# Performance work log

Hardware: AMD Instinct MI355X
Metric: run time of the kernel (lower is better)

## Reference

```python
import jax, jax.numpy as jnp
import numpy as np

# ---- static configuration (mirrors init_kwargs) ----
B, V, C, NH, HD = 1, 6, 256, 8, 32     # batch, views, embed, heads, head_dim
Z, L, P = 4, 4, 2                       # z-ref points, fmap levels, ref points
BEV_H, BEV_W = 80, 80
Q = BEV_H * BEV_W
IMG_H, IMG_W = 480, 800
LEVEL_SHAPES = [(60, 100), (30, 50), (15, 25), (8, 13)]
S = sum(h * w for h, w in LEVEL_SHAPES)
RES = 0.512
OFFSET_SCALE = 1.0
FF = 512


def layer_norm(x, g, b):
    m = jnp.mean(x, -1, keepdims=True)
    v = jnp.var(x, -1, keepdims=True)
    return (x - m) / jnp.sqrt(v + 1e-5) * g + b


def _bev_grid():
    xs = (jnp.arange(BEV_W) + 0.5) / BEV_W
    ys = (jnp.arange(BEV_H) + 0.5) / BEV_H
    gy, gx = jnp.meshgrid(ys, xs, indexing='ij')
    ref = jnp.stack([gx.reshape(-1), gy.reshape(-1)], -1)        # (Q,2) normalized xy
    world = (ref - 0.5) * jnp.array([BEV_W * RES, BEV_H * RES])  # (Q,2) ego-frame meters
    return ref, world


def deform_sample(value, H, W, loc):
    """Bilinear sampling. value: (N, H*W, NH, HD); loc: (N, Qn, NH, PP, 2) in [0,1].
    Returns (N, Qn, NH, PP, HD); out-of-bounds samples contribute zero."""
    v = jnp.moveaxis(value, 2, 1)                                # (N, NH, HW, HD)
    x = loc[..., 0] * W - 0.5
    y = loc[..., 1] * H - 0.5
    x0 = jnp.floor(x); y0 = jnp.floor(y)
    lx, ly = x - x0, y - y0
    x0 = x0.astype(jnp.int32); y0 = y0.astype(jnp.int32)
    gather = jax.vmap(jax.vmap(lambda vt, it: vt[it]))           # over (N, NH)
    def corner(xi, yi, w):
        ok = ((xi >= 0) & (xi < W) & (yi >= 0) & (yi < H)).astype(value.dtype)
        idx = jnp.clip(yi, 0, H - 1) * W + jnp.clip(xi, 0, W - 1)
        g = gather(v, jnp.moveaxis(idx, 2, 1))                   # (N,NH,Qn,PP,HD)
        return jnp.moveaxis(g, 1, 2) * (w * ok)[..., None]
    return (corner(x0, y0, (1 - lx) * (1 - ly)) + corner(x0 + 1, y0, lx * (1 - ly))
            + corner(x0, y0 + 1, (1 - lx) * ly) + corner(x0 + 1, y0 + 1, lx * ly))


def _forward(bev_queries, bev_histories, multiscale_fmaps, transition_matrices, z_refs,
             cam_proj_matrices, Wv_t, Woff_t, boff_t, Ww_t, bw_t, Wo_t, bo_t, ln1_g, ln1_b,
             Wv_s, Woff_s, boff_s, Ww_s, bw_s, Wo_s, bo_s, ln2_g, ln2_b,
             W1, b1, W2, b2, ln3_g, ln3_b):
    ref, world = _bev_grid()
    q = bev_queries
    # ---------- temporal self-attention (deformable over current + warped history) ----------
    vcur = (q @ Wv_t).reshape(B, Q, NH, HD)
    vhist = (bev_histories @ Wv_t).reshape(B, Q, NH, HD)
    off_t = (q @ Woff_t + boff_t).reshape(B, Q, NH, 2, P, 2) * OFFSET_SCALE
    w_t = jax.nn.softmax((q @ Ww_t + bw_t).reshape(B, Q, NH, 2 * P), -1).reshape(B, Q, NH, 2, P)
    ext = jnp.array([BEV_W * RES, BEV_H * RES], jnp.float32)
    wh = jnp.concatenate([world, jnp.ones((Q, 1), jnp.float32)], -1)     # (Q,3)
    warped = jnp.einsum('bij,qj->bqi', transition_matrices, wh)          # (B,Q,3)
    ref_hist = warped[..., :2] / warped[..., 2:3] / ext + 0.5            # (B,Q,2)
    norm_bev = jnp.array([BEV_W, BEV_H], jnp.float32)
    loc_c = ref[None, :, None, None, :] + off_t[:, :, :, 0] / norm_bev
    loc_h = ref_hist[:, :, None, None, :] + off_t[:, :, :, 1] / norm_bev
    s_c = deform_sample(vcur, BEV_H, BEV_W, loc_c)                       # (B,Q,NH,P,HD)
    s_h = deform_sample(vhist, BEV_H, BEV_W, loc_h)
    out_t = (jnp.einsum('bqhp,bqhpd->bqhd', w_t[:, :, :, 0], s_c)
             + jnp.einsum('bqhp,bqhpd->bqhd', w_t[:, :, :, 1], s_h))
    out1 = out_t.reshape(B, Q, C) @ Wo_t + bo_t
    out2 = layer_norm(out1 + q, ln1_g, ln1_b)
    # ---------- spatial cross-attention (multi-view multi-scale deformable) ----------
    val = (multiscale_fmaps @ Wv_s).reshape(B * V, S, NH, HD)
    pts = jnp.concatenate([
        jnp.broadcast_to(world[:, None, :], (Q, Z, 2)),
        jnp.broadcast_to(z_refs[None, :, None], (Q, Z, 1)),
        jnp.ones((Q, Z, 1), jnp.float32)], -1)                           # (Q,Z,4) homogeneous
    uvd = jnp.einsum('vij,qzj->vqzi', cam_proj_matrices, pts)            # (V,Q,Z,3)
    d = uvd[..., 2]
    un = uvd[..., 0] / jnp.maximum(d, 1e-5) / IMG_W
    vn = uvd[..., 1] / jnp.maximum(d, 1e-5) / IMG_H
    valid = ((d > 1e-5) & (un >= 0) & (un <= 1) & (vn >= 0) & (vn <= 1)).astype(q.dtype)
    refuv = jnp.stack([un, vn], -1)                                      # (V,Q,Z,2)
    off_s = (out2 @ Woff_s + boff_s).reshape(B, Q, NH, Z, L, P, 2) * OFFSET_SCALE
    w_s = jax.nn.softmax((out2 @ Ww_s + bw_s).reshape(B, Q, NH, Z * L * P), -1)
    w_s = w_s.reshape(B, Q, NH, Z, L, P)
    acc = jnp.zeros((B, Q, NH, HD), q.dtype)
    start = 0
    for l, (Hl, Wl) in enumerate(LEVEL_SHAPES):
        vl = val[:, start:start + Hl * Wl]
        start += Hl * Wl
        loc = (refuv[None, :, :, None, :, None, :]
               + off_s[:, None, :, :, :, l] / jnp.array([Wl, Hl], jnp.float32))
        loc = jnp.broadcast_to(loc, (B, V, Q, NH, Z, P, 2)).reshape(B * V, Q, NH, Z * P, 2)
        samp = deform_sample(vl, Hl, Wl, loc).reshape(B, V, Q, NH, Z, P, HD)
        wl = w_s[:, None, :, :, :, l] * valid[None, :, :, None, :, None]
        acc = acc + jnp.einsum('bvqhzp,bvqhzpd->bqhd', wl, samp)
    count = jnp.maximum(valid.sum((0, 2)), 1.0)                          # (Q,) hit count
    out3 = (acc / count[None, :, None, None]).reshape(B, Q, C) @ Wo_s + bo_s
    out4 = layer_norm(out3 + out2, ln2_g, ln2_b)
    # ---------- feed-forward ----------
    out5 = jax.nn.relu(out4 @ W1 + b1) @ W2 + b2
    return layer_norm(out5 + out4, ln3_g, ln3_b)


def setup_inputs() -> dict:
    key = jax.random.key(0)
    ks = iter(jax.random.split(key, 40))
    def rn(shape, s=1.0):
        return jax.random.normal(next(ks), shape, jnp.float32) * s
    sc = 1.0 / float(np.sqrt(C))
    inp = {}
    inp['bev_queries'] = rn((B, Q, C), 0.1)
    inp['bev_histories'] = rn((B, Q, C), 0.1)
    inp['multiscale_fmaps'] = rn((B, V, S, C), 0.1)
    th = 0.02
    T = np.array([[np.cos(th), -np.sin(th), 0.5],
                  [np.sin(th), np.cos(th), 0.1],
                  [0.0, 0.0, 1.0]], np.float32)
    inp['transition_matrices'] = jnp.tile(jnp.asarray(T)[None], (B, 1, 1))
    inp['z_refs'] = jnp.linspace(-5.0, 3.0, Z).astype(jnp.float32)
    K = np.array([[400.0, 0.0, IMG_W / 2], [0.0, 400.0, IMG_H / 2], [0.0, 0.0, 1.0]], np.float32)
    Ps = []
    for vi in range(V):
        a = 2 * np.pi * vi / V
        Rt = np.zeros((3, 4), np.float32)
        Rt[0, :3] = [-np.sin(a), np.cos(a), 0.0]   # camera right
        Rt[1, :3] = [0.0, 0.0, -1.0]               # camera down
        Rt[2, :3] = [np.cos(a), np.sin(a), 0.0]    # camera forward
        Ps.append(K @ Rt)
    inp['cam_proj_matrices'] = jnp.asarray(np.stack(Ps))
    # temporal self-attention params
    inp['Wv_t'] = rn((C, C), sc)
    inp['Woff_t'] = rn((C, NH * 2 * P * 2), sc * 0.1)
    inp['boff_t'] = jnp.zeros((NH * 2 * P * 2,), jnp.float32)
    inp['Ww_t'] = rn((C, NH * 2 * P), sc)
    inp['bw_t'] = jnp.zeros((NH * 2 * P,), jnp.float32)
    inp['Wo_t'] = rn((C, C), sc)
    inp['bo_t'] = jnp.zeros((C,), jnp.float32)
    inp['ln1_g'] = jnp.ones((C,), jnp.float32)
    inp['ln1_b'] = jnp.zeros((C,), jnp.float32)
    # spatial cross-attention params
    inp['Wv_s'] = rn((C, C), sc)
    inp['Woff_s'] = rn((C, NH * Z * L * P * 2), sc * 0.1)
    inp['boff_s'] = jnp.zeros((NH * Z * L * P * 2,), jnp.float32)
    inp['Ww_s'] = rn((C, NH * Z * L * P), sc)
    inp['bw_s'] = jnp.zeros((NH * Z * L * P,), jnp.float32)
    inp['Wo_s'] = rn((C, C), sc)
    inp['bo_s'] = jnp.zeros((C,), jnp.float32)
    inp['ln2_g'] = jnp.ones((C,), jnp.float32)
    inp['ln2_b'] = jnp.zeros((C,), jnp.float32)
    # FFN params
    inp['W1'] = rn((C, FF), sc)
    inp['b1'] = jnp.zeros((FF,), jnp.float32)
    inp['W2'] = rn((FF, C), 1.0 / float(np.sqrt(FF)))
    inp['b2'] = jnp.zeros((C,), jnp.float32)
    inp['ln3_g'] = jnp.ones((C,), jnp.float32)
    inp['ln3_b'] = jnp.zeros((C,), jnp.float32)
    # static shape descriptors (treated as compile-time constants)
    inp['bev_spatial_shape'] = np.array([[BEV_H, BEV_W]], np.int64)
    inp['multiscale_fmap_shapes'] = np.array(LEVEL_SHAPES, np.int64)
    inp['img_spatial_shape'] = np.array([[IMG_H, IMG_W]], np.int64)
    return inp


def reference(bev_queries, bev_histories, multiscale_fmaps, transition_matrices, z_refs,
              cam_proj_matrices, Wv_t, Woff_t, boff_t, Ww_t, bw_t, Wo_t, bo_t, ln1_g, ln1_b,
              Wv_s, Woff_s, boff_s, Ww_s, bw_s, Wo_s, bo_s, ln2_g, ln2_b,
              W1, b1, W2, b2, ln3_g, ln3_b,
              bev_spatial_shape, multiscale_fmap_shapes, img_spatial_shape):
    return _forward(bev_queries, bev_histories, multiscale_fmaps, transition_matrices, z_refs,
                    cam_proj_matrices, Wv_t, Woff_t, boff_t, Ww_t, bw_t, Wo_t, bo_t, ln1_g, ln1_b,
                    Wv_s, Woff_s, boff_s, Ww_s, bw_s, Wo_s, bo_s, ln2_g, ln2_b,
                    W1, b1, W2, b2, ln3_g, ln3_b)
```

## Files before the change

### kernel.cpp

```cpp
#include <hip/hip_runtime.h>
#include <hip/hip_bf16.h>
#include <hip/hip_fp16.h>

typedef unsigned short u16;
typedef unsigned int u32;
typedef __attribute__((ext_vector_type(8))) _Float16 f16x8;
typedef __attribute__((ext_vector_type(4))) float f32x4;

#define Q_N  6400
#define S_N  7979
#define BEV  80

__device__ __forceinline__ float f16tof(u16 u) {
    __half h; *(u16*)&h = u; return __half2float(h);
}
__device__ __forceinline__ u16 ftof16(float f) {
    __half h = __float2half(f); return *(u16*)&h;
}

template <int AIN, int RELU, int OUTMODE, int SM4, int SM32>
__device__ __forceinline__ void gemm_body(
    const void* __restrict__ A, const u16* __restrict__ WT,
    const float* __restrict__ bias, const float* __restrict__ bias2,
    void* __restrict__ Cout, int M, int N, int K, int bx, int by,
// ... 60 lines not shown
        int col = n0 + wn + j * 16 + fr;
        if (bias2) bv[j] = (col < 512) ? bias[col] : bias2[col - 512];
        else       bv[j] = bias ? bias[col] : 0.f;
    }
    const bool do_sm4  = SM4 && (wn == 64);
    #pragma unroll
    for (int i = 0; i < 2; ++i) {
        #pragma unroll
        for (int r = 0; r < 4; ++r) {
            const int row = m0 + wm + i * 16 + g4r + r;
            float v0 = acc[i * 4 + 0][r] + bv[0];
            float v1 = acc[i * 4 + 1][r] + bv[1];
            float v2 = acc[i * 4 + 2][r] + bv[2];
            float v3 = acc[i * 4 + 3][r] + bv[3];
            if (RELU) {
                v0 = fmaxf(v0, 0.f); v1 = fmaxf(v1, 0.f);
                v2 = fmaxf(v2, 0.f); v3 = fmaxf(v3, 0.f);
            }
            if (SM4 && do_sm4) {
                float m0q = fmaxf(v0, __shfl_xor(v0, 1));
                m0q = fmaxf(m0q, __shfl_xor(m0q, 2));
                float e0 = __expf(v0 - m0q);
                float s0 = e0 + __shfl_xor(e0, 1);
                s0 += __shfl_xor(s0, 2);
                v0 = e0 / s0;
                float m1q = fmaxf(v1, __shfl_xor(v1, 1));
                m1q = fmaxf(m1q, __shfl_xor(m1q, 2));
                float e1 = __expf(v1 - m1q);
                float s1 = e1 + __shfl_xor(e1, 1);
                s1 += __shfl_xor(s1, 2);
                v1 = e1 / s1;
                v2 = 0.f; v3 = 0.f;
            }
            if (row < M) {
                const int colb = n0 + wn + fr;
                if (OUTMODE == 1) {
                    u16* cp = (u16*)Cout + (size_t)row * N;
                    cp[colb]      = ftof16(v0);
                    cp[colb + 16] = ftof16(v1);
                    cp[colb + 32] = ftof16(v2);
                    cp[colb + 48] = ftof16(v3);
                } else {
                    float* cp = (float*)Cout + (size_t)row * N;
                    cp[colb]      = v0;
                    cp[colb + 16] = v1;
                    cp[colb + 32] = v2;
                    cp[colb + 48] = v3;
                }
            }
        }
    }
}

__global__ __launch_bounds__(256) void fused3_k(
    const float* __restrict__ fmaps, const float* __restrict__ q, const float* __restrict__ hist,
    const u16* __restrict__ Wv_s_h, const u16* __restrict__ Wv_t_h,
    const u16* __restrict__ Wc_h, const float* __restrict__ bc,
    u16* __restrict__ val_f16, u16* __restrict__ vcur, u16* __restrict__ vhist,
    float* __restrict__ owt)
{
    __shared__ u16 Ah[64 * 40], Wh[128 * 40];
    const int b = blockIdx.x;
    if (b < 1498) {
        gemm_body<0, 0, 1, 0, 0>(fmaps, Wv_s_h, nullptr, nullptr, val_f16,
                                 47874, 256, 256, b & 1, b >> 1, Ah, Wh);
    } else if (b < 1698) {
        int l = b - 1498;
        gemm_body<0, 0, 1, 0, 0>(q, Wv_t_h, nullptr, nullptr, vcur,
                                 6400, 256, 256, l & 1, l >> 1, Ah, Wh);
    } else if (b < 1898) {
        int l = b - 1698;
        gemm_body<0, 0, 1, 0, 0>(hist, Wv_t_h, nullptr, nullptr, vhist,
                                 6400, 256, 256, l & 1, l >> 1, Ah, Wh);
    } else {
        int l = b - 1898;
        gemm_body<0, 0, 0, 1, 0>(q, Wc_h, bc, nullptr, owt,
                                 6400, 128, 256, 0, l, Ah, Wh);
    }
}

template <int AIN, int RELU, int OUTMODE, int SM32, int STATS, int LNA>
__global__ __launch_bounds__(256, 4) void cgemm_k(
    const void* __restrict__ A, const u16* __restrict__ WT,
    const float* __restrict__ bias, const float* __restrict__ bias2,
    const float* __restrict__ res, float* __restrict__ rstat,
    const float* __restrict__ lng, const float* __restrict__ lnb,
    float* __restrict__ aux,
    void* __restrict__ Cout, int M, int N, int K)
{
    __shared__ u16 As[2][32 * 40];
    __shared__ u16 Wsh[2][64 * 40];
    const int tid  = threadIdx.x;
    const int lane = tid & 63;
    const int wave = tid >> 6;
    const int wm = (wave >> 1) * 16, wn = (wave & 1) * 32;
    const int fr = lane & 15, g = lane >> 4;
    const int nx = gridDim.x;
    const int nwg = nx * gridDim.y;
    const int o = blockIdx.y * nx + blockIdx.x;
    const int flat = (o & 7) * (nwg >> 3) + (o >> 3);
    const int bx = flat % nx, by = flat / nx;
    const int m0 = by * 32, n0 = bx * 64;
    const int ar = tid >> 3, ak = (tid & 7) * 4;
    const int wr = tid >> 2, wk = (tid & 3) * 8;
    const int NS = K >> 5;

    f32x4 acc[2] = {(f32x4)(0.f), (f32x4)(0.f)};

    const float* apf = (const float*)A + (size_t)(m0 + ar) * K + ak;
    const u16*  aph  = (const u16*)A + (size_t)(m0 + ar) * K + ak;
    const u16*  wp   = WT + (size_t)(n0 + wr) * K + wk;

    const float* rp = nullptr;
    float* auxp = nullptr;
    float mean = 0.f, rstd = 0.f;
    if (LNA) {
        rp = res + (size_t)(m0 + ar) * 256 + ak;
        if (bx == 0) auxp = aux + (size_t)(m0 + ar) * 256 + ak;
        const float sm = rstat[m0 + ar];
        const float sq = rstat[Q_N + m0 + ar];
        mean = sm * (1.f / 256.f);
        rstd = rsqrtf(sq * (1.f / 256.f) - mean * mean + 1e-5f);
    }

    if (AIN == 0) {
        float4 v = *(const float4*)apf;
        if (LNA) {
            float4 rr = *(const float4*)rp;
            float4 gg = *(const float4*)(lng + ak);
            float4 bb = *(const float4*)(lnb + ak);
            v.x = (v.x + rr.x - mean) * rstd * gg.x + bb.x;
            v.y = (v.y + rr.y - mean) * rstd * gg.y + bb.y;
            v.z = (v.z + rr.z - mean) * rstd * gg.z + bb.z;
            v.w = (v.w + rr.w - mean) * rstd * gg.w + bb.w;
            if (auxp) *(float4*)auxp = v;
        }
        u16 hb[4];
        hb[0] = ftof16(v.x); hb[1] = ftof16(v.y); hb[2] = ftof16(v.z); hb[3] = ftof16(v.w);
        *(ushort4*)&As[0][ar * 40 + ak] = *(ushort4*)&hb[0];
    } else {
        *(uint2*)&As[0][ar * 40 + ak] = *(const uint2*)aph;
    }
    *(uint4*)&Wsh[0][wr * 40 + wk] = *(const uint4*)wp;
    __syncthreads();

    for (int s = 0; s < NS; ++s) {
        float4 av; float4 rv; uint2 au; uint4 wv;
        const bool pf = (s + 1) < NS;
        if (pf) {
            if (AIN == 0) {
                av = *(const float4*)(apf + (s + 1) * 32);
                if (LNA) rv = *(const float4*)(rp + (s + 1) * 32);
            } else {
                au = *(const uint2*)(aph + (s + 1) * 32);
            }
            wv = *(const uint4*)(wp + (s + 1) * 32);
        }
        const int b = s & 1;
        f16x8 fa  = *(const f16x8*)&As[b][(wm + fr) * 40 + g * 8];
        f16x8 fw0 = *(const f16x8*)&Wsh[b][(wn + fr) * 40 + g * 8];
        f16x8 fw1 = *(const f16x8*)&Wsh[b][(wn + 16 + fr) * 40 + g * 8];
        acc[0] = __builtin_amdgcn_mfma_f32_16x16x32_f16(fa, fw0, acc[0], 0, 0, 0);
        acc[1] = __builtin_amdgcn_mfma_f32_16x16x32_f16(fa, fw1, acc[1], 0, 0, 0);
        if (pf) {
            const int nb = b ^ 1;
            if (AIN == 0) {
                if (LNA) {
                    const int ko = ak + (s + 1) * 32;
                    float4 gg = *(const float4*)(lng + ko);
                    float4 bb = *(const float4*)(lnb + ko);
                    av.x = (av.x + rv.x - mean) * rstd * gg.x + bb.x;
                    av.y = (av.y + rv.y - mean) * rstd * gg.y + bb.y;
                    av.z = (av.z + rv.z - mean) * rstd * gg.z + bb.z;
                    av.w = (av.w + rv.w - mean) * rstd * gg.w + bb.w;
                    if (auxp) *(float4*)(auxp + (s + 1) * 32) = av;
                }
                u16 hb[4];
                hb[0] = ftof16(av.x); hb[1] = ftof16(av.y);
                hb[2] = ftof16(av.z); hb[3] = ftof16(av.w);
                *(ushort4*)&As[nb][ar * 40 + ak] = *(ushort4*)&hb[0];
            } else {
                *(uint2*)&As[nb][ar * 40 + ak] = au;
            }
            *(uint4*)&Wsh[nb][wr * 40 + wk] = wv;
        }
        __syncthreads();
    }

    const int c0g = n0 + wn + fr, c1g = c0g + 16;
    float bv0, bv1;
    if (bias2) {
        bv0 = (c0g < 512) ? bias[c0g] : bias2[c0g - 512];
        bv1 = (c1g < 512) ? bias[c1g] : bias2[c1g - 512];
    } else {
        bv0 = bias ? bias[c0g] : 0.f;
        bv1 = bias ? bias[c1g] : 0.f;
    }
    const bool do_sm32 = SM32 && ((n0 + wn) >= 512);
    #pragma unroll
    for (int r = 0; r < 4; ++r) {
        const int row = m0 + wm + g * 4 + r;
        float v0 = acc[0][r] + bv0;
        float v1 = acc[1][r] + bv1;
        if (RELU) { v0 = fmaxf(v0, 0.f); v1 = fmaxf(v1, 0.f); }
        if (SM32 && do_sm32) {
            float ma = fmaxf(v0, v1);
            ma = fmaxf(ma, __shfl_xor(ma, 1));
            ma = fmaxf(ma, __shfl_xor(ma, 2));
            ma = fmaxf(ma, __shfl_xor(ma, 4));
            ma = fmaxf(ma, __shfl_xor(ma, 8));
            float e0 = __expf(v0 - ma), e1 = __expf(v1 - ma);
            float sa = e0 + e1;
            sa += __shfl_xor(sa, 1);
            sa += __shfl_xor(sa, 2);
            sa += __shfl_xor(sa, 4);
            sa += __shfl_xor(sa, 8);
            float ia = 1.f / sa;
            v0 = e0 * ia; v1 = e1 * ia;
        }
        if (STATS) {
            float t0 = v0 + res[(size_t)row * 256 + c0g];
            float t1 = v1 + res[(size_t)row * 256 + c1g];
            float s1v = t0 + t1;
            float s2v = t0 * t0 + t1 * t1;
            s1v += __shfl_xor(s1v, 1); s1v += __shfl_xor(s1v, 2);
            s1v += __shfl_xor(s1v, 4); s1v += __shfl_xor(s1v, 8);
            s2v += __shfl_xor(s2v, 1); s2v += __shfl_xor(s2v, 2);
            s2v += __shfl_xor(s2v, 4); s2v += __shfl_xor(s2v, 8);
            if (fr == 0) {
                atomicAdd(&rstat[row], s1v);
                atomicAdd(&rstat[Q_N + row], s2v);
            }
        }
        if (row < M) {
            if (OUTMODE == 1) {
                u16* cp = (u16*)Cout + (size_t)row * N;
                cp[c0g] = ftof16(v0);
                cp[c1g] = ftof16(v1);
            } else {
                float* cp = (float*)Cout + (size_t)row * N;
                cp[c0g] = v0;
                cp[c1g] = v1;
            }
        }
    }
}

__global__ __launch_bounds__(256) void wprep_k(
    const float* __restrict__ w0, const float* __restrict__ w1, const float* __restrict__ w2,
    const float* __restrict__ w3, const float* __restrict__ w4, const float* __restrict__ w5,
    const float* __restrict__ w6, const float* __restrict__ w7, u16* __restrict__ base,
    const float* __restrict__ Woff_t, const float* __restrict__ Ww_t,
    const float* __restrict__ boff_t, const float* __restrict__ bw_t,
    float* __restrict__ bc, float* __restrict__ st)
{
    const int b = blockIdx.x, tid = threadIdx.x;
    if (b >= 185) {
        st[(b - 185) * 256 + tid] = 0.f;
        return;
    }
    if (b == 184) {
        if (tid < 128) bc[tid] = (tid < 64) ? boff_t[tid] : (tid < 96 ? bw_t[tid - 64] : 0.f);
        return;
    }
    const int cum[10]  = {0, 16, 32, 48, 80, 96, 112, 144, 176, 184};
    const int Ks[9]    = {256, 256, 256, 256, 256, 256, 256, 512, 256};
    const int Ns[9]    = {256, 256, 256, 512, 256, 256, 512, 256, 128};
    const int hoff[9]  = {0, 65536, 131072, 196608, 327680, 393216, 458752, 589824, 720896};
    int seg = 0;
    #pragma unroll
    for (int s = 1; s < 9; ++s) if (b >= cum[s]) seg = s;
    const int K = Ks[seg], N = Ns[seg];
    const int t = b - cum[seg];
    const int ntn = N / 64;
    const int k0 = (t / ntn) * 64, n0 = (t % ntn) * 64;
    __shared__ float tile[64][65];
    const int rr = tid >> 2, cc = (tid & 3) * 16;
    if (seg < 8) {
        const float* W = seg == 0 ? w0 : seg == 1 ? w1 : seg == 2 ? w2 : seg == 3 ? w3 :
                         seg == 4 ? w4 : seg == 5 ? w5 : seg == 6 ? w6 : w7;
        #pragma unroll
        for (int c = 0; c < 4; ++c) {
            float4 v = *(const float4*)(W + (size_t)(k0 + rr) * N + n0 + cc + c * 4);
            tile[rr][cc + c * 4 + 0] = v.x;
            tile[rr][cc + c * 4 + 1] = v.y;
            tile[rr][cc + c * 4 + 2] = v.z;
            tile[rr][cc + c * 4 + 3] = v.w;
        }
    } else {
        #pragma unroll
        for (int i = 0; i < 16; ++i) {
            int n = n0 + cc + i, k = k0 + rr;
            float v = (n < 64) ? Woff_t[k * 64 + n] : (n < 96 ? Ww_t[k * 32 + n - 64] : 0.f);
            tile[rr][cc + i] = v;
        }
    }
    __syncthreads();
    const int nr = tid >> 2, kc = (tid & 3) * 16;
    u16 hb[16];
    #pragma unroll
    for (int i = 0; i < 16; ++i) hb[i] = ftof16(tile[kc + i][nr]);
    u16* hp = base + hoff[seg] + (size_t)(n0 + nr) * K + k0 + kc;
    *(ushort4*)(hp + 0)  = *(ushort4*)&hb[0];
    *(ushort4*)(hp + 4)  = *(ushort4*)&hb[4];
    *(ushort4*)(hp + 8)  = *(ushort4*)&hb[8];
    *(ushort4*)(hp + 12) = *(ushort4*)&hb[12];
}

__global__ __launch_bounds__(256) void ln_k(
    const float* __restrict__ x, const float* __restrict__ res,
    const float* __restrict__ g, const float* __restrict__ b,
    float* __restrict__ out)
{
    const int row = blockIdx.x, t = threadIdx.x;
    const size_t idx = (size_t)row * 256 + t;
    float v = x[idx] + res[idx];
    float s = v, ss = v * v;
    #pragma unroll
    for (int o = 32; o > 0; o >>= 1) {
        s += __shfl_down(s, o);
        ss += __shfl_down(ss, o);
    }
    __shared__ float red[8];
    __shared__ float mv[2];
    const int wv = t >> 6, ln = t & 63;
    if (ln == 0) { red[wv] = s; red[4 + wv] = ss; }
    __syncthreads();
    if (t == 0) {
        float S = red[0] + red[1] + red[2] + red[3];
        float SS = red[4] + red[5] + red[6] + red[7];
        float mean = S * (1.f / 256.f);
        float var = SS * (1.f / 256.f) - mean * mean;
        mv[0] = mean;
        mv[1] = rsqrtf(var + 1e-5f);
    }
    __syncthreads();
    out[idx] = (v - mv[0]) * mv[1] * g[t] + b[t];
}

__device__ __forceinline__ float4 bilin4h(const u16* __restrict__ v, int H, int W,
                                          float x, float y, int chb)
{
    float xf = floorf(x), yf = floorf(y);
    int x0 = (int)xf, y0 = (int)yf;
    int x1 = x0 + 1, y1 = y0 + 1;
    float fx = x - xf, fy = y - yf;
    float w00 = (1.f - fx) * (1.f - fy), w10 = fx * (1.f - fy);
    float w01 = (1.f - fx) * fy,         w11 = fx * fy;
    bool xi0 = (x0 >= 0) && (x0 < W);
    bool xi1 = (x1 >= 0) && (x1 < W);
    bool yi0 = (y0 >= 0) && (y0 < H);
    bool yi1 = (y1 >= 0) && (y1 < H);
    float4 r = make_float4(0.f, 0.f, 0.f, 0.f);
    #define CORNER(xi, yi, xx, yy, ww)                                           \
        if ((yi) && (xi)) {                                                      \
            uint2 u = *(const uint2*)(v + ((size_t)(yy) * W + (xx)) * 256 + chb);\
            float2 f0 = __half22float2(*(const __half2*)&u.x);                   \
            float2 f1 = __half22float2(*(const __half2*)&u.y);                   \
            r.x += (ww) * f0.x; r.y += (ww) * f0.y;                              \
            r.z += (ww) * f1.x; r.w += (ww) * f1.y;                              \
        }
    CORNER(xi0, yi0, x0, y0, w00)
    CORNER(xi1, yi0, x1, y0, w10)
    CORNER(xi0, yi1, x0, y1, w01)
    CORNER(xi1, yi1, x1, y1, w11)
    #undef CORNER
    return r;
}

__global__ __launch_bounds__(256) void temporal_k(
    const u16* __restrict__ vcur, const u16* __restrict__ vhist,
    const float* __restrict__ ow,
    const float* __restrict__ Tm, float* __restrict__ outt)
{
    const int b = blockIdx.x;
    const int q = (b & 7) * 800 + (b >> 3);
    const int tid = threadIdx.x;
    const int c4 = tid & 63, rep = tid >> 6;
    const int br = rep >> 1, p = rep & 1;
    const int h = c4 >> 3;
    const int chb = h * 32 + (c4 & 7) * 4;
    const int jx = q % BEV, iy = q / BEV;
    const float refx = (jx + 0.5f) / 80.f;
    const float refy = (iy + 0.5f) / 80.f;
    const float wx = (refx - 0.5f) * 40.96f;
    const float wy = (refy - 0.5f) * 40.96f;
    float bx, by;
    const u16* v;
    if (br == 0) { v = vcur; bx = refx; by = refy; }
    else {
        float h0 = Tm[0] * wx + Tm[1] * wy + Tm[2];
        float h1 = Tm[3] * wx + Tm[4] * wy + Tm[5];
        float h2 = Tm[6] * wx + Tm[7] * wy + Tm[8];
        v = vhist;
        bx = h0 / h2 / 40.96f + 0.5f;
        by = h1 / h2 / 40.96f + 0.5f;
    }
    const float* owq = ow + (size_t)q * 128;
    int ob = h * 8 + br * 4 + p * 2;
    float lx = bx + owq[ob] * (1.f / 80.f);
    float ly = by + owq[ob + 1] * (1.f / 80.f);
    float wgt = owq[64 + h * 4 + br * 2 + p];
    float4 sv = bilin4h(v, BEV, BEV, lx * 80.f - 0.5f, ly * 80.f - 0.5f, chb);
    __shared__ float4 s_acc[4][64];
    s_acc[rep][c4] = make_float4(wgt * sv.x, wgt * sv.y, wgt * sv.z, wgt * sv.w);
    __syncthreads();
    if (rep == 0) {
        float4 a = s_acc[0][c4], b2 = s_acc[1][c4], c = s_acc[2][c4], d = s_acc[3][c4];
        float4 o = make_float4(a.x + b2.x + c.x + d.x, a.y + b2.y + c.y + d.y,
                               a.z + b2.z + c.z + d.z, a.w + b2.w + c.w + d.w);
        *(float4*)(outt + (size_t)q * 256 + c4 * 4) = o;
    }
}

__global__ __launch_bounds__(256) void spatial_k(
    const u16* __restrict__ val, const u16* __restrict__ ow,
    const float* __restrict__ cam, const float* __restrict__ zrefs,
    float* __restrict__ out)
{
    const int b = blockIdx.x;
    const int q = (b & 7) * 800 + (b >> 3);
    const int tid = threadIdx.x;
    const int lane = tid & 63, wave = tid >> 6;
    const int hw = lane >> 5, lh = lane & 31;
    const int slot = wave * 2 + hw;
    const int h = lh >> 2, chb = h * 32 + (lh & 3) * 8;
    __shared__ float s_un[24], s_vn[24], s_ok[24];
    __shared__ int s_list[24];
    __shared__ int s_n;
    __shared__ float s_cnt;
    __shared__ float s_ox[256], s_oy[256], s_wt[256];
    __shared__ float s_part[8][256];
    const int jx = q % BEV, iy = q / BEV;
    const float wx = ((jx + 0.5f) / 80.f - 0.5f) * 40.96f;
    const float wy = ((iy + 0.5f) / 80.f - 0.5f) * 40.96f;
    if (tid < 24) {
        int v = tid >> 2, zz = tid & 3;
        float zr = zrefs[zz];
        const float* P = cam + v * 12;
        float u0 = P[0] * wx + P[1] * wy + P[2] * zr + P[3];
        float u1 = P[4] * wx + P[5] * wy + P[6] * zr + P[7];
        float dd = P[8] * wx + P[9] * wy + P[10] * zr + P[11];
        float dm = fmaxf(dd, 1e-5f);
        float un = u0 / dm / 800.f;
        float vn = u1 / dm / 480.f;
        bool ok = (dd > 1e-5f) && (un >= 0.f) && (un <= 1.f) && (vn >= 0.f) && (vn <= 1.f);
        s_un[tid] = un; s_vn[tid] = vn; s_ok[tid] = ok ? 1.f : 0.f;
    }
    {
        const u16* owq = ow + (size_t)q * 768;
        #pragma unroll
        for (int rep = 0; rep < 2; ++rep) {
            int flat = tid + rep * 256;
            int hh = flat >> 6, rem = flat & 63;
            int zz = rem >> 4, ll = (rem >> 2) & 3, pp = (rem >> 1) & 1, xy = rem & 1;
            int dst = (zz * 8 + ll * 2 + pp) * 8 + hh;
            float v = f16tof(owq[flat]);
            if (xy) s_oy[dst] = v; else s_ox[dst] = v;
        }
        int hh = tid >> 5, rem = tid & 31;
        s_wt[rem * 8 + hh] = f16tof(owq[512 + tid]);
    }
    __syncthreads();
    if (tid == 0) {
        int n = 0; float c = 0.f;
// ... 93 lines not shown
    const float* Tm     = (const float*)d_in[3];
    const float* zrefs  = (const float*)d_in[4];
    const float* cam    = (const float*)d_in[5];
    const float* Woff_t = (const float*)d_in[7];
    const float* boff_t = (const float*)d_in[8];
    const float* Ww_t   = (const float*)d_in[9];
    const float* bw_t   = (const float*)d_in[10];
    const float* bo_t   = (const float*)d_in[12];
    const float* ln1g   = (const float*)d_in[13];
    const float* ln1b   = (const float*)d_in[14];
    const float* boff_s = (const float*)d_in[17];
    const float* bw_s   = (const float*)d_in[19];
    const float* bo_s   = (const float*)d_in[21];
    const float* ln2g   = (const float*)d_in[22];
    const float* ln2b   = (const float*)d_in[23];
    const float* b1     = (const float*)d_in[25];
    const float* b2     = (const float*)d_in[27];
    const float* ln3g   = (const float*)d_in[28];
    const float* ln3b   = (const float*)d_in[29];

    float* ws    = (float*)d_ws;
    float* r0    = ws;
    float* r1    = ws + 1638400;
    float* owt   = ws + 3276800;
    float* r4    = ws + 4096000;
    u16*  r5u    = (u16*)(ws + 5734400);
    float* of4   = ws + 8192000;
    u16*  valbuf = (u16*)(ws + 9830400);
    u16*  vcur   = (u16*)(ws + 15958272);
    u16*  vhist  = (u16*)(ws + 16777472);
    u16*  wtab   = (u16*)(ws + 17596672);
    float* st1   = ws + 17973504;
    float* st2   = ws + 17986304;
    float* bc    = ws + 18350336;

    u16* hidden = valbuf;
    u16* Wv_t_h = wtab + 0;
    u16* Wo_t_h = wtab + 65536;
    u16* Wv_s_h = wtab + 131072;
    u16* Comb_h = wtab + 196608;
    u16* Wo_s_h = wtab + 393216;
    u16* W1_h   = wtab + 458752;
    u16* W2_h   = wtab + 589824;
    u16* Wc_h   = wtab + 720896;

    dim3 blk(256);
    auto gc = [](int M, int N) { return dim3((unsigned)(N / 64), (unsigned)((M + 31) / 32)); };

    wprep_k<<<dim3(285), blk, 0, stream>>>(
        (const float*)d_in[6], (const float*)d_in[11], (const float*)d_in[15],
        (const float*)d_in[16], (const float*)d_in[18], (const float*)d_in[20],
        (const float*)d_in[24], (const float*)d_in[26], wtab,
        Woff_t, Ww_t, boff_t, bw_t, bc, st1);
    fused3_k<<<dim3(1998), blk, 0, stream>>>(
        fmaps, q, hist, Wv_s_h, Wv_t_h, Wc_h, bc,
        valbuf, vcur, vhist, owt);
    temporal_k<<<dim3(6400), blk, 0, stream>>>(vcur, vhist, owt, Tm, r4);
    cgemm_k<0,0,0,0,1,0><<<gc(6400, 256), blk, 0, stream>>>(
        r4, Wo_t_h, bo_t, nullptr, q, st1, nullptr, nullptr, nullptr,
        r0, 6400, 256, 256);
    cgemm_k<0,0,1,1,0,1><<<gc(6400, 768), blk, 0, stream>>>(
        r0, Comb_h, boff_s, bw_s, q, st1, ln1g, ln1b, r1,
        r5u, 6400, 768, 256);
    spatial_k<<<dim3(6400), blk, 0, stream>>>(valbuf, r5u, cam, zrefs, r0);
    cgemm_k<0,0,0,0,1,0><<<gc(6400, 256), blk, 0, stream>>>(
        r0, Wo_s_h, bo_s, nullptr, r1, st2, nullptr, nullptr, nullptr,
        r4, 6400, 256, 256);
    cgemm_k<0,1,1,0,0,1><<<gc(6400, 512), blk, 0, stream>>>(
        r4, W1_h, b1, nullptr, r1, st2, ln2g, ln2b, of4,
        hidden, 6400, 512, 256);
    cgemm_k<1,0,0,0,0,0><<<gc(6400, 256), blk, 0, stream>>>(
        hidden, W2_h, b2, nullptr, nullptr, nullptr, nullptr, nullptr, nullptr,
        r0, 6400, 256, 512);
    ln_k<<<dim3(6400), blk, 0, stream>>>(r0, of4, ln3g, ln3b, (float*)d_out);
}
```

Before: 302.8 us.

## Overlap spatial value projection with temporal sampling; register-prefetch cgemm K-loop

Result: slower. 388.6 us (+28.3%).

```diff
diff --git a/kernel.cpp b/kernel.cpp
--- a/kernel.cpp
+++ b/kernel.cpp
@@ -136,290 +136,26 @@
     }
 }
 
-__global__ __launch_bounds__(256) void fused3_k(
-    const float* __restrict__ fmaps, const float* __restrict__ q, const float* __restrict__ hist,
-    const u16* __restrict__ Wv_s_h, const u16* __restrict__ Wv_t_h,
-    const u16* __restrict__ Wc_h, const float* __restrict__ bc,
-    u16* __restrict__ val_f16, u16* __restrict__ vcur, u16* __restrict__ vhist,
-    float* __restrict__ owt)
+__global__ __launch_bounds__(256) void fused3a_k(
+    const float* __restrict__ q, const float* __restrict__ hist,
+    const u16* __restrict__ Wv_t_h, const u16* __restrict__ Wc_h,
+    const float* __restrict__ bc,
+    u16* __restrict__ vcur, u16* __restrict__ vhist, float* __restrict__ owt)
 {
     __shared__ u16 Ah[64 * 40], Wh[128 * 40];
     const int b = blockIdx.x;
-    if (b < 1498) {
-        gemm_body<0, 0, 1, 0, 0>(fmaps, Wv_s_h, nullptr, nullptr, val_f16,
-                                 47874, 256, 256, b & 1, b >> 1, Ah, Wh);
-    } else if (b < 1698) {
-        int l = b - 1498;
+    if (b < 200) {
         gemm_body<0, 0, 1, 0, 0>(q, Wv_t_h, nullptr, nullptr, vcur,
-                                 6400, 256, 256, l & 1, l >> 1, Ah, Wh);
-    } else if (b < 1898) {
-        int l = b - 1698;
+                                 6400, 256, 256, b & 1, b >> 1, Ah, Wh);
+    } else if (b < 400) {
+        int l = b - 200;
         gemm_body<0, 0, 1, 0, 0>(hist, Wv_t_h, nullptr, nullptr, vhist,
                                  6400, 256, 256, l & 1, l >> 1, Ah, Wh);
     } else {
-        int l = b - 1898;
+        int l = b - 400;
         gemm_body<0, 0, 0, 1, 0>(q, Wc_h, bc, nullptr, owt,
                                  6400, 128, 256, 0, l, Ah, Wh);
     }
-}
-
-template <int AIN, int RELU, int OUTMODE, int SM32, int STATS, int LNA>
-__global__ __launch_bounds__(256, 4) void cgemm_k(
-    const void* __restrict__ A, const u16* __restrict__ WT,
-    const float* __restrict__ bias, const float* __restrict__ bias2,
-    const float* __restrict__ res, float* __restrict__ rstat,
-    const float* __restrict__ lng, const float* __restrict__ lnb,
-    float* __restrict__ aux,
-    void* __restrict__ Cout, int M, int N, int K)
-{
-    __shared__ u16 As[2][32 * 40];
-    __shared__ u16 Wsh[2][64 * 40];
-    const int tid  = threadIdx.x;
-    const int lane = tid & 63;
-    const int wave = tid >> 6;
-    const int wm = (wave >> 1) * 16, wn = (wave & 1) * 32;
-    const int fr = lane & 15, g = lane >> 4;
-    const int nx = gridDim.x;
-    const int nwg = nx * gridDim.y;
-    const int o = blockIdx.y * nx + blockIdx.x;
-    const int flat = (o & 7) * (nwg >> 3) + (o >> 3);
-    const int bx = flat % nx, by = flat / nx;
-    const int m0 = by * 32, n0 = bx * 64;
-    const int ar = tid >> 3, ak = (tid & 7) * 4;
-    const int wr = tid >> 2, wk = (tid & 3) * 8;
-    const int NS = K >> 5;
-
-    f32x4 acc[2] = {(f32x4)(0.f), (f32x4)(0.f)};
-
-    const float* apf = (const float*)A + (size_t)(m0 + ar) * K + ak;
-    const u16*  aph  = (const u16*)A + (size_t)(m0 + ar) * K + ak;
-    const u16*  wp   = WT + (size_t)(n0 + wr) * K + wk;
-
-    const float* rp = nullptr;
-    float* auxp = nullptr;
-    float mean = 0.f, rstd = 0.f;
-    if (LNA) {
-        rp = res + (size_t)(m0 + ar) * 256 + ak;
-        if (bx == 0) auxp = aux + (size_t)(m0 + ar) * 256 + ak;
-        const float sm = rstat[m0 + ar];
-        const float sq = rstat[Q_N + m0 + ar];
-        mean = sm * (1.f / 256.f);
-        rstd = rsqrtf(sq * (1.f / 256.f) - mean * mean + 1e-5f);
-    }
-
-    if (AIN == 0) {
-        float4 v = *(const float4*)apf;
-        if (LNA) {
-            float4 rr = *(const float4*)rp;
-            float4 gg = *(const float4*)(lng + ak);
-            float4 bb = *(const float4*)(lnb + ak);
-            v.x = (v.x + rr.x - mean) * rstd * gg.x + bb.x;
-            v.y = (v.y + rr.y - mean) * rstd * gg.y + bb.y;
-            v.z = (v.z + rr.z - mean) * rstd * gg.z + bb.z;
-            v.w = (v.w + rr.w - mean) * rstd * gg.w + bb.w;
-            if (auxp) *(float4*)auxp = v;
-        }
-        u16 hb[4];
-        hb[0] = ftof16(v.x); hb[1] = ftof16(v.y); hb[2] = ftof16(v.z); hb[3] = ftof16(v.w);
-        *(ushort4*)&As[0][ar * 40 + ak] = *(ushort4*)&hb[0];
-    } else {
-        *(uint2*)&As[0][ar * 40 + ak] = *(const uint2*)aph;
-    }
-    *(uint4*)&Wsh[0][wr * 40 + wk] = *(const uint4*)wp;
-    __syncthreads();
-
-    for (int s = 0; s < NS; ++s) {
-        float4 av; float4 rv; uint2 au; uint4 wv;
-        const bool pf = (s + 1) < NS;
-        if (pf) {
-            if (AIN == 0) {
-                av = *(const float4*)(apf + (s + 1) * 32);
-                if (LNA) rv = *(const float4*)(rp + (s + 1) * 32);
-            } else {
-                au = *(const uint2*)(aph + (s + 1) * 32);
-            }
-            wv = *(const uint4*)(wp + (s + 1) * 32);
-        }
-        const int b = s & 1;
-        f16x8 fa  = *(const f16x8*)&As[b][(wm + fr) * 40 + g * 8];
-        f16x8 fw0 = *(const f16x8*)&Wsh[b][(wn + fr) * 40 + g * 8];
-        f16x8 fw1 = *(const f16x8*)&Wsh[b][(wn + 16 + fr) * 40 + g * 8];
-        acc[0] = __builtin_amdgcn_mfma_f32_16x16x32_f16(fa, fw0, acc[0], 0, 0, 0);
-        acc[1] = __builtin_amdgcn_mfma_f32_16x16x32_f16(fa, fw1, acc[1], 0, 0, 0);
-        if (pf) {
-            const int nb = b ^ 1;
-            if (AIN == 0) {
-                if (LNA) {
-                    const int ko = ak + (s + 1) * 32;
-                    float4 gg = *(const float4*)(lng + ko);
-                    float4 bb = *(const float4*)(lnb + ko);
-                    av.x = (av.x + rv.x - mean) * rstd * gg.x + bb.x;
-                    av.y = (av.y + rv.y - mean) * rstd * gg.y + bb.y;
-                    av.z = (av.z + rv.z - mean) * rstd * gg.z + bb.z;
-                    av.w = (av.w + rv.w - mean) * rstd * gg.w + bb.w;
-                    if (auxp) *(float4*)(auxp + (s + 1) * 32) = av;
-                }
-                u16 hb[4];
-                hb[0] = ftof16(av.x); hb[1] = ftof16(av.y);
-                hb[2] = ftof16(av.z); hb[3] = ftof16(av.w);
-                *(ushort4*)&As[nb][ar * 40 + ak] = *(ushort4*)&hb[0];
-            } else {
-                *(uint2*)&As[nb][ar * 40 + ak] = au;
-            }
-            *(uint4*)&Wsh[nb][wr * 40 + wk] = wv;
-        }
-        __syncthreads();
-    }
-
-    const int c0g = n0 + wn + fr, c1g = c0g + 16;
-    float bv0, bv1;
-    if (bias2) {
-        bv0 = (c0g < 512) ? bias[c0g] : bias2[c0g - 512];
-        bv1 = (c1g < 512) ? bias[c1g] : bias2[c1g - 512];
-    } else {
-        bv0 = bias ? bias[c0g] : 0.f;
-        bv1 = bias ? bias[c1g] : 0.f;
-    }
-    const bool do_sm32 = SM32 && ((n0 + wn) >= 512);
-    #pragma unroll
-    for (int r = 0; r < 4; ++r) {
-        const int row = m0 + wm + g * 4 + r;
-        float v0 = acc[0][r] + bv0;
-        float v1 = acc[1][r] + bv1;
-        if (RELU) { v0 = fmaxf(v0, 0.f); v1 = fmaxf(v1, 0.f); }
-        if (SM32 && do_sm32) {
-            float ma = fmaxf(v0, v1);
-            ma = fmaxf(ma, __shfl_xor(ma, 1));
-            ma = fmaxf(ma, __shfl_xor(ma, 2));
-            ma = fmaxf(ma, __shfl_xor(ma, 4));
-            ma = fmaxf(ma, __shfl_xor(ma, 8));
-            float e0 = __expf(v0 - ma), e1 = __expf(v1 - ma);
-            float sa = e0 + e1;
-            sa += __shfl_xor(sa, 1);
-            sa += __shfl_xor(sa, 2);
-            sa += __shfl_xor(sa, 4);
-            sa += __shfl_xor(sa, 8);
-            float ia = 1.f / sa;
-            v0 = e0 * ia; v1 = e1 * ia;
-        }
-        if (STATS) {
-            float t0 = v0 + res[(size_t)row * 256 + c0g];
-            float t1 = v1 + res[(size_t)row * 256 + c1g];
-            float s1v = t0 + t1;
-            float s2v = t0 * t0 + t1 * t1;
-            s1v += __shfl_xor(s1v, 1); s1v += __shfl_xor(s1v, 2);
-            s1v += __shfl_xor(s1v, 4); s1v += __shfl_xor(s1v, 8);
-            s2v += __shfl_xor(s2v, 1); s2v += __shfl_xor(s2v, 2);
-            s2v += __shfl_xor(s2v, 4); s2v += __shfl_xor(s2v, 8);
-            if (fr == 0) {
-                atomicAdd(&rstat[row], s1v);
-                atomicAdd(&rstat[Q_N + row], s2v);
-            }
-        }
-        if (row < M) {
-            if (OUTMODE == 1) {
-                u16* cp = (u16*)Cout + (size_t)row * N;
-                cp[c0g] = ftof16(v0);
-                cp[c1g] = ftof16(v1);
-            } else {
-                float* cp = (float*)Cout + (size_t)row * N;
-                cp[c0g] = v0;
-                cp[c1g] = v1;
-            }
-        }
-    }
-}
-
-__global__ __launch_bounds__(256) void wprep_k(
-    const float* __restrict__ w0, const float* __restrict__ w1, const float* __restrict__ w2,
-    const float* __restrict__ w3, const float* __restrict__ w4, const float* __restrict__ w5,
-    const float* __restrict__ w6, const float* __restrict__ w7, u16* __restrict__ base,
-    const float* __restrict__ Woff_t, const float* __restrict__ Ww_t,
-    const float* __restrict__ boff_t, const float* __restrict__ bw_t,
-    float* __restrict__ bc, float* __restrict__ st)
-{
-    const int b = blockIdx.x, tid = threadIdx.x;
-    if (b >= 185) {
-        st[(b - 185) * 256 + tid] = 0.f;
-        return;
-    }
-    if (b == 184) {
-        if (tid < 128) bc[tid] = (tid < 64) ? boff_t[tid] : (tid < 96 ? bw_t[tid - 64] : 0.f);
-        return;
-    }
-    const int cum[10]  = {0, 16, 32, 48, 80, 96, 112, 144, 176, 184};
-    const int Ks[9]    = {256, 256, 256, 256, 256, 256, 256, 512, 256};
-    const int Ns[9]    = {256, 256, 256, 512, 256, 256, 512, 256, 128};
-    const int hoff[9]  = {0, 65536, 131072, 196608, 327680, 393216, 458752, 589824, 720896};
-    int seg = 0;
-    #pragma unroll
-    for (int s = 1; s < 9; ++s) if (b >= cum[s]) seg = s;
-    const int K = Ks[seg], N = Ns[seg];
-    const int t = b - cum[seg];
-    const int ntn = N / 64;
-    const int k0 = (t / ntn) * 64, n0 = (t % ntn) * 64;
-    __shared__ float tile[64][65];
-    const int rr = tid >> 2, cc = (tid & 3) * 16;
-    if (seg < 8) {
-        const float* W = seg == 0 ? w0 : seg == 1 ? w1 : seg == 2 ? w2 : seg == 3 ? w3 :
-                         seg == 4 ? w4 : seg == 5 ? w5 : seg == 6 ? w6 : w7;
-        #pragma unroll
-        for (int c = 0; c < 4; ++c) {
-            float4 v = *(const float4*)(W + (size_t)(k0 + rr) * N + n0 + cc + c * 4);
-            tile[rr][cc + c * 4 + 0] = v.x;
-            tile[rr][cc + c * 4 + 1] = v.y;
-            tile[rr][cc + c * 4 + 2] = v.z;
-            tile[rr][cc + c * 4 + 3] = v.w;
-        }
-    } else {
-        #pragma unroll
-        for (int i = 0; i < 16; ++i) {
-            int n = n0 + cc + i, k = k0 + rr;
-            float v = (n < 64) ? Woff_t[k * 64 + n] : (n < 96 ? Ww_t[k * 32 + n - 64] : 0.f);
-            tile[rr][cc + i] = v;
-        }
-    }
-    __syncthreads();
-    const int nr = tid >> 2, kc = (tid & 3) * 16;
-    u16 hb[16];
-    #pragma unroll
-    for (int i = 0; i < 16; ++i) hb[i] = ftof16(tile[kc + i][nr]);
-    u16* hp = base + hoff[seg] + (size_t)(n0 + nr) * K + k0 + kc;
-    *(ushort4*)(hp + 0)  = *(ushort4*)&hb[0];
-    *(ushort4*)(hp + 4)  = *(ushort4*)&hb[4];
-    *(ushort4*)(hp + 8)  = *(ushort4*)&hb[8];
-    *(ushort4*)(hp + 12) = *(ushort4*)&hb[12];
-}
-
-__global__ __launch_bounds__(256) void ln_k(
-    const float* __restrict__ x, const float* __restrict__ res,
-    const float* __restrict__ g, const float* __restrict__ b,
-    float* __restrict__ out)
-{
-    const int row = blockIdx.x, t = threadIdx.x;
-    const size_t idx = (size_t)row * 256 + t;
-    float v = x[idx] + res[idx];
-    float s = v, ss = v * v;
-    #pragma unroll
-    for (int o = 32; o > 0; o >>= 1) {
-        s += __shfl_down(s, o);
-        ss += __shfl_down(ss, o);
-    }
-    __shared__ float red[8];
-    __shared__ float mv[2];
-    const int wv = t >> 6, ln = t & 63;
-    if (ln == 0) { red[wv] = s; red[4 + wv] = ss; }
-    __syncthreads();
-    if (t == 0) {
-        float S = red[0] + red[1] + red[2] + red[3];
-        float SS = red[4] + red[5] + red[6] + red[7];
-        float mean = S * (1.f / 256.f);
-        float var = SS * (1.f / 256.f) - mean * mean;
-        mv[0] = mean;
-        mv[1] = rsqrtf(var + 1e-5f);
-    }
-    __syncthreads();
-    out[idx] = (v - mv[0]) * mv[1] * g[t] + b[t];
 }
 
 __device__ __forceinline__ float4 bilin4h(const u16* __restrict__ v, int H, int W,
@@ -452,12 +188,11 @@
     return r;
 }
 
-__global__ __launch_bounds__(256) void temporal_k(
+__device__ __forceinline__ void temporal_body(
     const u16* __restrict__ vcur, const u16* __restrict__ vhist,
-    const float* __restrict__ ow,
-    const float* __restrict__ Tm, float* __restrict__ outt)
-{
-    const int b = blockIdx.x;
+    const float* __restrict__ ow, const float* __restrict__ Tm,
+    float* __restrict__ outt, int b, char* smem)
+{
     const int q = (b & 7) * 800 + (b >> 3);
     const int tid = threadIdx.x;
     const int c4 = tid & 63, rep = tid >> 6;
@@ -486,7 +221,7 @@
     float ly = by + owq[ob + 1] * (1.f / 80.f);
     float wgt = owq[64 + h * 4 + br * 2 + p];
     float4 sv = bilin4h(v, BEV, BEV, lx * 80.f - 0.5f, ly * 80.f - 0.5f, chb);
-    __shared__ float4 s_acc[4][64];
+    float4 (*s_acc)[64] = (float4 (*)[64])smem;
     s_acc[rep][c4] = make_float4(wgt * sv.x, wgt * sv.y, wgt * sv.z, wgt * sv.w);
     __syncthreads();
     if (rep == 0) {
@@ -495,6 +230,289 @@
                                a.z + b2.z + c.z + d.z, a.w + b2.w + c.w + d.w);
         *(float4*)(outt + (size_t)q * 256 + c4 * 4) = o;
     }
+}
+
+__global__ __launch_bounds__(256) void valtemp_k(
+    const float* __restrict__ fmaps, const u16* __restrict__ Wv_s_h,
+    u16* __restrict__ val_f16,
+    const u16* __restrict__ vcur, const u16* __restrict__ vhist,
+    const float* __restrict__ ow, const float* __restrict__ Tm,
+    float* __restrict__ outt)
+{
+    __shared__ __align__(16) char smem[15360];
+    const int b = blockIdx.x;
+    if (b < 1498) {
+        u16* Ah = (u16*)smem;
+        u16* Wh = (u16*)(smem + 5120);
+        gemm_body<0, 0, 1, 0, 0>(fmaps, Wv_s_h, nullptr, nullptr, val_f16,
+                                 47874, 256, 256, b & 1, b >> 1, Ah, Wh);
+    } else {
+        temporal_body(vcur, vhist, ow, Tm, outt, b - 1498, smem);
+    }
+}
+
+template <int AIN, int RELU, int OUTMODE, int SM32, int STATS, int LNA, int KK>
+__global__ __launch_bounds__(256, 4) void cgemm_k(
+    const void* __restrict__ A, const u16* __restrict__ WT,
+    const float* __restrict__ bias, const float* __restrict__ bias2,
+    const float* __restrict__ res, float* __restrict__ rstat,
+    const float* __restrict__ lng, const float* __restrict__ lnb,
+    float* __restrict__ aux,
+    void* __restrict__ Cout, int M, int N)
+{
+    constexpr int NS = KK >> 5;
+    constexpr int WD = (NS < 8) ? NS : 8;
+    constexpr int AD = LNA ? 4 : ((NS < 8) ? NS : 8);
+    __shared__ u16 As[2][32 * 40];
+    __shared__ u16 Wsh[2][64 * 40];
+    const int tid  = threadIdx.x;
+    const int lane = tid & 63;
+    const int wave = tid >> 6;
+    const int wm = (wave >> 1) * 16, wn = (wave & 1) * 32;
+    const int fr = lane & 15, g = lane >> 4;
+    const int nx = gridDim.x;
+    const int nwg = nx * gridDim.y;
+    const int o = blockIdx.y * nx + blockIdx.x;
+    const int flat = (o & 7) * (nwg >> 3) + (o >> 3);
+    const int bx = flat % nx, by = flat / nx;
+    const int m0 = by * 32, n0 = bx * 64;
+    const int ar = tid >> 3, ak = (tid & 7) * 4;
+    const int wr = tid >> 2, wk = (tid & 3) * 8;
+
+    f32x4 acc[2] = {(f32x4)(0.f), (f32x4)(0.f)};
+
+    const float* apf = (const float*)A + (size_t)(m0 + ar) * KK + ak;
+    const u16*  aph  = (const u16*)A + (size_t)(m0 + ar) * KK + ak;
+    const u16*  wp   = WT + (size_t)(n0 + wr) * KK + wk;
+
+    const float* rp = nullptr;
+    float* auxp = nullptr;
+    float mean = 0.f, rstd = 0.f;
+    if (LNA) {
+        rp = res + (size_t)(m0 + ar) * 256 + ak;
+        if (bx == 0) auxp = aux + (size_t)(m0 + ar) * 256 + ak;
+        const float sm = rstat[m0 + ar];
+        const float sq = rstat[Q_N + m0 + ar];
+        mean = sm * (1.f / 256.f);
+        rstd = rsqrtf(sq * (1.f / 256.f) - mean * mean + 1e-5f);
+    }
+
+    uint4 wR[WD];
+    #pragma unroll
+    for (int s = 0; s < WD; ++s) wR[s] = *(const uint4*)(wp + s * 32);
+    float4 aF[(AIN == 0) ? AD : 1];
+    float4 rF[(AIN == 0 && LNA) ? AD : 1];
+    uint2  aH[(AIN == 1) ? AD : 1];
+    #pragma unroll
+    for (int s = 0; s < AD; ++s) {
+        if (AIN == 0) {
+            aF[s] = *(const float4*)(apf + s * 32);
+            if (LNA) rF[s] = *(const float4*)(rp + s * 32);
+        } else {
+            aH[s] = *(const uint2*)(aph + s * 32);
+        }
+    }
+
+    auto stageA = [&](int t, int buf) {
+        if (AIN == 0) {
+            float4 v = aF[t % AD];
+            if (LNA) {
+                float4 rr = rF[t % AD];
+                const int ko = ak + t * 32;
+                float4 gg = *(const float4*)(lng + ko);
+                float4 bb = *(const float4*)(lnb + ko);
+                v.x = (v.x + rr.x - mean) * rstd * gg.x + bb.x;
+                v.y = (v.y + rr.y - mean) * rstd * gg.y + bb.y;
+                v.z = (v.z + rr.z - mean) * rstd * gg.z + bb.z;
+                v.w = (v.w + rr.w - mean) * rstd * gg.w + bb.w;
+                if (auxp) *(float4*)(auxp + t * 32) = v;
+            }
+            u16 hb[4];
+            hb[0] = ftof16(v.x); hb[1] = ftof16(v.y);
+            hb[2] = ftof16(v.z); hb[3] = ftof16(v.w);
+            *(ushort4*)&As[buf][ar * 40 + ak] = *(ushort4*)&hb[0];
+        } else {
+            *(uint2*)&As[buf][ar * 40 + ak] = aH[t % AD];
+        }
+    };
+
+    stageA(0, 0);
+    *(uint4*)&Wsh[0][wr * 40 + wk] = wR[0];
+    __syncthreads();
+
+    #pragma unroll
+    for (int s = 0; s < NS; ++s) {
+        if (s + WD < NS) wR[s % WD] = *(const uint4*)(wp + (s + WD) * 32);
+        if (AIN == 0) {
+            if (s + AD < NS) {
+                aF[s % AD] = *(const float4*)(apf + (s + AD) * 32);
+                if (LNA) rF[s % AD] = *(const float4*)(rp + (s + AD) * 32);
+            }
+        } else {
+            if (s + AD < NS) aH[s % AD] = *(const uint2*)(aph + (s + AD) * 32);
+        }
+        if (s + 1 < NS) {
+            stageA(s + 1, (s + 1) & 1);
+            *(uint4*)&Wsh[(s + 1) & 1][wr * 40 + wk] = wR[(s + 1) % WD];
+        }
+        const int b = s & 1;
+        f16x8 fa  = *(const f16x8*)&As[b][(wm + fr) * 40 + g * 8];
+        f16x8 fw0 = *(const f16x8*)&Wsh[b][(wn + fr) * 40 + g * 8];
+        f16x8 fw1 = *(const f16x8*)&Wsh[b][(wn + 16 + fr) * 40 + g * 8];
+        acc[0] = __builtin_amdgcn_mfma_f32_16x16x32_f16(fa, fw0, acc[0], 0, 0, 0);
+        acc[1] = __builtin_amdgcn_mfma_f32_16x16x32_f16(fa, fw1, acc[1], 0, 0, 0);
+        __syncthreads();
+    }
+
+    const int c0g = n0 + wn + fr, c1g = c0g + 16;
+    float bv0, bv1;
+    if (bias2) {
+        bv0 = (c0g < 512) ? bias[c0g] : bias2[c0g - 512];
+        bv1 = (c1g < 512) ? bias[c1g] : bias2[c1g - 512];
+    } else {
+        bv0 = bias ? bias[c0g] : 0.f;
+        bv1 = bias ? bias[c1g] : 0.f;
+    }
+    const bool do_sm32 = SM32 && ((n0 + wn) >= 512);
+    #pragma unroll
+    for (int r = 0; r < 4; ++r) {
+        const int row = m0 + wm + g * 4 + r;
+        float v0 = acc[0][r] + bv0;
+        float v1 = acc[1][r] + bv1;
+        if (RELU) { v0 = fmaxf(v0, 0.f); v1 = fmaxf(v1, 0.f); }
+        if (SM32 && do_sm32) {
+            float ma = fmaxf(v0, v1);
+            ma = fmaxf(ma, __shfl_xor(ma, 1));
+            ma = fmaxf(ma, __shfl_xor(ma, 2));
+            ma = fmaxf(ma, __shfl_xor(ma, 4));
+            ma = fmaxf(ma, __shfl_xor(ma, 8));
+            float e0 = __expf(v0 - ma), e1 = __expf(v1 - ma);
+            float sa = e0 + e1;
+            sa += __shfl_xor(sa, 1);
+            sa += __shfl_xor(sa, 2);
+            sa += __shfl_xor(sa, 4);
+            sa += __shfl_xor(sa, 8);
+            float ia = 1.f / sa;
+            v0 = e0 * ia; v1 = e1 * ia;
+        }
+        if (STATS) {
+            float t0 = v0 + res[(size_t)row * 256 + c0g];
+            float t1 = v1 + res[(size_t)row * 256 + c1g];
+            float s1v = t0 + t1;
+            float s2v = t0 * t0 + t1 * t1;
+            s1v += __shfl_xor(s1v, 1); s1v += __shfl_xor(s1v, 2);
+            s1v += __shfl_xor(s1v, 4); s1v += __shfl_xor(s1v, 8);
+            s2v += __shfl_xor(s2v, 1); s2v += __shfl_xor(s2v, 2);
+            s2v += __shfl_xor(s2v, 4); s2v += __shfl_xor(s2v, 8);
+            if (fr == 0) {
+                atomicAdd(&rstat[row], s1v);
+                atomicAdd(&rstat[Q_N + row], s2v);
+            }
+        }
+        if (row < M) {
+            if (OUTMODE == 1) {
+                u16* cp = (u16*)Cout + (size_t)row * N;
+                cp[c0g] = ftof16(v0);
+                cp[c1g] = ftof16(v1);
+            } else {
+                float* cp = (float*)Cout + (size_t)row * N;
+                cp[c0g] = v0;
+                cp[c1g] = v1;
+            }
+        }
+    }
+}
+
+__global__ __launch_bounds__(256) void wprep_k(
+    const float* __restrict__ w0, const float* __restrict__ w1, const float* __restrict__ w2,
+    const float* __restrict__ w3, const float* __restrict__ w4, const float* __restrict__ w5,
+    const float* __restrict__ w6, const float* __restrict__ w7, u16* __restrict__ base,
+    const float* __restrict__ Woff_t, const float* __restrict__ Ww_t,
+    const float* __restrict__ boff_t, const float* __restrict__ bw_t,
+    float* __restrict__ bc, float* __restrict__ st)
+{
+    const int b = blockIdx.x, tid = threadIdx.x;
+    if (b >= 185) {
+        st[(b - 185) * 256 + tid] = 0.f;
+        return;
+    }
+    if (b == 184) {
+        if (tid < 128) bc[tid] = (tid < 64) ? boff_t[tid] : (tid < 96 ? bw_t[tid - 64] : 0.f);
+        return;
+    }
+    const int cum[10]  = {0, 16, 32, 48, 80, 96, 112, 144, 176, 184};
+    const int Ks[9]    = {256, 256, 256, 256, 256, 256, 256, 512, 256};
+    const int Ns[9]    = {256, 256, 256, 512, 256, 256, 512, 256, 128};
+    const int hoff[9]  = {0, 65536, 131072, 196608, 327680, 393216, 458752, 589824, 720896};
+    int seg = 0;
+    #pragma unroll
+    for (int s = 1; s < 9; ++s) if (b >= cum[s]) seg = s;
+    const int K = Ks[seg], N = Ns[seg];
+    const int t = b - cum[seg];
+    const int ntn = N / 64;
+    const int k0 = (t / ntn) * 64, n0 = (t % ntn) * 64;
+    __shared__ float tile[64][65];
+    const int rr = tid >> 2, cc = (tid & 3) * 16;
+    if (seg < 8) {
+        const float* W = seg == 0 ? w0 : seg == 1 ? w1 : seg == 2 ? w2 : seg == 3 ? w3 :
+                         seg == 4 ? w4 : seg == 5 ? w5 : seg == 6 ? w6 : w7;
+        #pragma unroll
+        for (int c = 0; c < 4; ++c) {
+            float4 v = *(const float4*)(W + (size_t)(k0 + rr) * N + n0 + cc + c * 4);
+            tile[rr][cc + c * 4 + 0] = v.x;
+            tile[rr][cc + c * 4 + 1] = v.y;
+            tile[rr][cc + c * 4 + 2] = v.z;
+            tile[rr][cc + c * 4 + 3] = v.w;
+        }
+    } else {
+        #pragma unroll
+        for (int i = 0; i < 16; ++i) {
+            int n = n0 + cc + i, k = k0 + rr;
+            float v = (n < 64) ? Woff_t[k * 64 + n] : (n < 96 ? Ww_t[k * 32 + n - 64] : 0.f);
+            tile[rr][cc + i] = v;
+        }
+    }
+    __syncthreads();
+    const int nr = tid >> 2, kc = (tid & 3) * 16;
+    u16 hb[16];
+    #pragma unroll
+    for (int i = 0; i < 16; ++i) hb[i] = ftof16(tile[kc + i][nr]);
+    u16* hp = base + hoff[seg] + (size_t)(n0 + nr) * K + k0 + kc;
+    *(ushort4*)(hp + 0)  = *(ushort4*)&hb[0];
+    *(ushort4*)(hp + 4)  = *(ushort4*)&hb[4];
+    *(ushort4*)(hp + 8)  = *(ushort4*)&hb[8];
+    *(ushort4*)(hp + 12) = *(ushort4*)&hb[12];
+}
+
+__global__ __launch_bounds__(256) void ln_k(
+    const float* __restrict__ x, const float* __restrict__ res,
+    const float* __restrict__ g, const float* __restrict__ b,
+    float* __restrict__ out)
+{
+    const int row = blockIdx.x, t = threadIdx.x;
+    const size_t idx = (size_t)row * 256 + t;
+    float v = x[idx] + res[idx];
+    float s = v, ss = v * v;
+    #pragma unroll
+    for (int o = 32; o > 0; o >>= 1) {
+        s += __shfl_down(s, o);
+        ss += __shfl_down(ss, o);
+    }
+    __shared__ float red[8];
+    __shared__ float mv[2];
+    const int wv = t >> 6, ln = t & 63;
+    if (ln == 0) { red[wv] = s; red[4 + wv] = ss; }
+    __syncthreads();
+    if (t == 0) {
+        float S = red[0] + red[1] + red[2] + red[3];
+        float SS = red[4] + red[5] + red[6] + red[7];
+        float mean = S * (1.f / 256.f);
+        float var = SS * (1.f / 256.f) - mean * mean;
+        mv[0] = mean;
+        mv[1] = rsqrtf(var + 1e-5f);
+    }
+    __syncthreads();
+    out[idx] = (v - mv[0]) * mv[1] * g[t] + b[t];
 }
 
 __global__ __launch_bounds__(256) void spatial_k(
@@ -694,25 +712,25 @@
         (const float*)d_in[16], (const float*)d_in[18], (const float*)d_in[20],
         (const float*)d_in[24], (const float*)d_in[26], wtab,
         Woff_t, Ww_t, boff_t, bw_t, bc, st1);
-    fused3_k<<<dim3(1998), blk, 0, stream>>>(
-        fmaps, q, hist, Wv_s_h, Wv_t_h, Wc_h, bc,
-        valbuf, vcur, vhist, owt);
-    temporal_k<<<dim3(6400), blk, 0, stream>>>(vcur, vhist, owt, Tm, r4);
-    cgemm_k<0,0,0,0,1,0><<<gc(6400, 256), blk, 0, stream>>>(
+    fused3a_k<<<dim3(500), blk, 0, stream>>>(
+        q, hist, Wv_t_h, Wc_h, bc, vcur, vhist, owt);
+    valtemp_k<<<dim3(7898), blk, 0, stream>>>(
+        fmaps, Wv_s_h, valbuf, vcur, vhist, owt, Tm, r4);
+    cgemm_k<0,0,0,0,1,0,256><<<gc(6400, 256), blk, 0, stream>>>(
         r4, Wo_t_h, bo_t, nullptr, q, st1, nullptr, nullptr, nullptr,
-        r0, 6400, 256, 256);
-    cgemm_k<0,0,1,1,0,1><<<gc(6400, 768), blk, 0, stream>>>(
+        r0, 6400, 256);
+    cgemm_k<0,0,1,1,0,1,256><<<gc(6400, 768), blk, 0, stream>>>(
         r0, Comb_h, boff_s, bw_s, q, st1, ln1g, ln1b, r1,
-        r5u, 6400, 768, 256);
+        r5u, 6400, 768);
     spatial_k<<<dim3(6400), blk, 0, stream>>>(valbuf, r5u, cam, zrefs, r0);
-    cgemm_k<0,0,0,0,1,0><<<gc(6400, 256), blk, 0, stream>>>(
+    cgemm_k<0,0,0,0,1,0,256><<<gc(6400, 256), blk, 0, stream>>>(
         r0, Wo_s_h, bo_s, nullptr, r1, st2, nullptr, nullptr, nullptr,
-        r4, 6400, 256, 256);
-    cgemm_k<0,1,1,0,0,1><<<gc(6400, 512), blk, 0, stream>>>(
+        r4, 6400, 256);
+    cgemm_k<0,1,1,0,0,1,256><<<gc(6400, 512), blk, 0, stream>>>(
         r4, W1_h, b1, nullptr, r1, st2, ln2g, ln2b, of4,
-        hidden, 6400, 512, 256);
-    cgemm_k<1,0,0,0,0,0><<<gc(6400, 256), blk, 0, stream>>>(
+        hidden, 6400, 512);
+    cgemm_k<1,0,0,0,0,0,512><<<gc(6400, 256), blk, 0, stream>>>(
         hidden, W2_h, b2, nullptr, nullptr, nullptr, nullptr, nullptr, nullptr,
-        r0, 6400, 256, 512);
+        r0, 6400, 256);
     ln_k<<<dim3(6400), blk, 0, stream>>>(r0, of4, ln3g, ln3b, (float*)d_out);
 }
```
